# Performance work log

Hardware: AMD Instinct MI355X
Metric: run time of the kernel (lower is better)

The kernel has to match this reference:

```python
import jax, jax.numpy as jnp
import numpy as np

B, S, D = 32, 4096, 64          # batch, max seq len, input_dim
P, STRIDE, H = 8, 4, 512        # patch_size, patch_stride, hidden_size
T = (S - P) // STRIDE + 1       # static max token count (sample 0 has length S)
EPS = 1e-6


def setup_inputs() -> dict:
    key = jax.random.key(0)
    k1, k2, k3 = jax.random.split(key, 3)
    x = jax.random.normal(k1, (B, S, D), dtype=jnp.float32)
    lengths = jax.random.randint(k2, (B,), P, S + 1)
    lengths = lengths.at[0].set(S)  # at least one full-length sample -> max_tokens == T
    W = jax.random.normal(k3, (P * D, H), dtype=jnp.float32) / np.sqrt(P * D)
    b = jnp.zeros((H,), dtype=jnp.float32)
    scale = jnp.ones((H,), dtype=jnp.float32)  # RMSNorm scale
    return {"x": x, "lengths": lengths, "W": W, "b": b, "scale": scale}


def _patch(x, lengths):
    # number of tokens per sample: len(range(0, max(L-P+1, 1), STRIDE))
    n_tok = jnp.where(lengths >= P, (lengths - P) // STRIDE + 1, 1)  # [B]
    # gather positions for every (token, within-patch) slot
    pos = jnp.arange(T)[:, None] * STRIDE + jnp.arange(P)[None, :]   # [T, P]
    tokens = x[:, pos, :]                                            # [B, T, P, D]
    valid = (pos[None, :, :] < lengths[:, None, None]) \
          & (jnp.arange(T)[None, :, None] < n_tok[:, None, None])    # [B, T, P]
    tokens = jnp.where(valid[..., None], tokens, 0.0)
    return tokens.reshape(B, T, P * D), n_tok


def reference(x, lengths, W, b, scale):
    tokens, token_lengths = _patch(x, lengths)        # [B, T, P*D], [B]
    h = tokens @ W + b                                # proj -> [B, T, H]
    rms = jnp.sqrt(jnp.mean(h * h, axis=-1, keepdims=True) + EPS)
    hidden = h / rms * scale                          # RMSNorm
    return hidden, token_lengths, tokens
```

## Files before the change

kernel.cpp:

```cpp
#include <hip/hip_runtime.h>
#include <hip/hip_bf16.h>

constexpr int Bc = 32, Sc = 4096, Dc = 64, Pc = 8, STRIDEc = 4, Hc = 512;
constexpr int Tc = (Sc - Pc) / STRIDEc + 1;
constexpr int Kc = Pc * Dc;
constexpr float EPSc = 1e-6f;
constexpr int APITCH = 40;

typedef __bf16 bf16x8 __attribute__((ext_vector_type(8)));
typedef unsigned short ushort8 __attribute__((ext_vector_type(8)));
typedef float f32x4 __attribute__((ext_vector_type(4)));

__device__ __forceinline__ int n_tok_of(int len) {
    return (len >= Pc) ? ((len - Pc) / STRIDEc + 1) : 1;
}

__device__ __forceinline__ unsigned short f2bf(float f) {
    unsigned u = __builtin_bit_cast(unsigned, f);
    u = (u + 0x7FFFu + ((u >> 16) & 1u)) >> 16;
    return (unsigned short)u;
}
__device__ __forceinline__ unsigned pk2bf(float lo, float hi) {
    return (unsigned)f2bf(lo) | ((unsigned)f2bf(hi) << 16);
}

#define GLOAD_LDS16(gp, lp)                                                   \
    __builtin_amdgcn_global_load_lds(                                         \
        (const __attribute__((address_space(1))) void*)(gp),                  \
        (__attribute__((address_space(3))) void*)(lp), 16, 0, 0)

__global__ __launch_bounds__(256) void prep_kernel(
        const float* __restrict__ W, const int* __restrict__ lengths,
        unsigned short* __restrict__ Wfrag, float* __restrict__ out_tl) {
    __shared__ float tile[32][33];
    const int k0 = blockIdx.x * 32, n0 = blockIdx.y * 32;
    const int r = threadIdx.x >> 3, c = (threadIdx.x & 7) * 4;
    const float4 v = *(const float4*)(W + (size_t)(k0 + r) * Hc + n0 + c);
    tile[c + 0][r] = v.x;
    tile[c + 1][r] = v.y;
    tile[c + 2][r] = v.z;
    tile[c + 3][r] = v.w;
    __syncthreads();
    ushort4 o;
    o.x = f2bf(tile[r][c + 0]);
    o.y = f2bf(tile[r][c + 1]);
    o.z = f2bf(tile[r][c + 2]);
    o.w = f2bf(tile[r][c + 3]);
    const int n   = n0 + r;
    const int kk  = k0 + c;
    const int st  = kk >> 5;
    const int kg  = (kk >> 3) & 3;
    const int j   = kk & 7;
    const int slot = kg ^ ((n >> 1) & 3);
    const size_t off = (size_t)st * 16384 + (size_t)n * 32 + slot * 8 + j;
    *(ushort4*)(Wfrag + off) = o;
    if (blockIdx.x == 0 && blockIdx.y == 0 && threadIdx.x < Bc)
        out_tl[threadIdx.x] = (float)n_tok_of(lengths[threadIdx.x]);
}

__global__ __launch_bounds__(256) void fused_kernel(
        const float* __restrict__ x, const int* __restrict__ lengths,
        const unsigned short* __restrict__ Wfrag, const float* __restrict__ bias,
        const float* __restrict__ scale, float* __restrict__ hidden,
        float* __restrict__ tokens) {
    const int b  = blockIdx.y;
    const int t0 = blockIdx.x * 64;
    const int len = lengths[b];
    const int ntok = n_tok_of(len);

    __shared__ unsigned short As[64 * APITCH];
    __shared__ unsigned short Bs[512 * 32];
    __shared__ float ssbuf[4][64];

    const int tid  = threadIdx.x;
    const int w    = tid >> 6;
    const int lane = tid & 63;
    const int l15  = lane & 15;
    const int quad = lane >> 4;

    f32x4 acc[4][8];
#pragma unroll
    for (int tt = 0; tt < 4; ++tt)
#pragma unroll
        for (int ct = 0; ct < 8; ++ct) acc[tt][ct] = (f32x4){0.f, 0.f, 0.f, 0.f};

    const float* xb   = x + (size_t)b * (Sc * Dc);
    float*       tokb = tokens + (size_t)b * Tc * Kc;

    const unsigned short* a_rd[4];
#pragma unroll
    for (int tt = 0; tt < 4; ++tt)
        a_rd[tt] = As + (tt * 16 + l15) * APITCH + quad * 8;
    const unsigned short* b_rd[8];
#pragma unroll
    for (int ct = 0; ct < 8; ++ct) {
        const int n = w * 128 + ct * 16 + l15;
        b_rd[ct] = Bs + n * 32 + (quad ^ ((n >> 1) & 3)) * 8;
    }

    for (int step = 0; step < 16; ++step) {
        const int k0 = step * 32;
        if (step) __syncthreads();

#pragma unroll
        for (int it = 0; it < 2; ++it) {
            const int l = tid + it * 256;
            const int r = l >> 3;
            const int c = (l & 7) * 4;
            const int t = t0 + r;
            const int kk = k0 + c;
            const int pos = t * STRIDEc + (kk >> 6);
            float4 v = make_float4(0.f, 0.f, 0.f, 0.f);
            if (t < ntok && pos < len)
                v = *(const float4*)(xb + (size_t)t * (STRIDEc * Dc) + kk);
            if (t < Tc)
                *(float4*)(tokb + (size_t)t * Kc + kk) = v;
            ushort4 h4;
            h4.x = f2bf(v.x); h4.y = f2bf(v.y); h4.z = f2bf(v.z); h4.w = f2bf(v.w);
            *(ushort4*)(As + r * APITCH + c) = h4;
        }

        const unsigned short* wstep = Wfrag + (size_t)step * 16384;
#pragma unroll
        for (int it = 0; it < 8; ++it) {
            const int cc = w * 8 + it;
            GLOAD_LDS16(wstep + (size_t)cc * 512 + lane * 8, Bs + cc * 512);
        }
        __syncthreads();

        bf16x8 btok[4];
#pragma unroll
        for (int tt = 0; tt < 4; ++tt)
            btok[tt] = __builtin_bit_cast(bf16x8, *(const ushort8*)a_rd[tt]);
#pragma unroll
        for (int ct = 0; ct < 8; ++ct) {
            const bf16x8 av = __builtin_bit_cast(bf16x8, *(const ushort8*)b_rd[ct]);
#pragma unroll
            for (int tt = 0; tt < 4; ++tt)
                acc[tt][ct] = __builtin_amdgcn_mfma_f32_16x16x32_bf16(
                    av, btok[tt], acc[tt][ct], 0, 0, 0);
        }
    }

    float ss[4] = {0.f, 0.f, 0.f, 0.f};
#pragma unroll
    for (int ct = 0; ct < 8; ++ct) {
        const f32x4 b4 = *(const f32x4*)(bias + w * 128 + ct * 16 + quad * 4);
#pragma unroll
        for (int tt = 0; tt < 4; ++tt) {
            f32x4 h = acc[tt][ct] + b4;
            acc[tt][ct] = h;
            ss[tt] += h[0] * h[0] + h[1] * h[1] + h[2] * h[2] + h[3] * h[3];
        }
    }
#pragma unroll
    for (int tt = 0; tt < 4; ++tt) {
        float s = ss[tt];
        s += __shfl_xor(s, 16);
        s += __shfl_xor(s, 32);
        if (quad == 0) ssbuf[w][tt * 16 + l15] = s;
    }
    __syncthreads();
    float rstd[4];
#pragma unroll
    for (int tt = 0; tt < 4; ++tt) {
        const int r = tt * 16 + l15;
        const float tot = ssbuf[0][r] + ssbuf[1][r] + ssbuf[2][r] + ssbuf[3][r];
        rstd[tt] = rsqrtf(tot * (1.0f / (float)Hc) + EPSc);
    }
#pragma unroll
    for (int ct = 0; ct < 8; ++ct) {
        const f32x4 s4 = *(const f32x4*)(scale + w * 128 + ct * 16 + quad * 4);
#pragma unroll
        for (int tt = 0; tt < 4; ++tt) {
            const int t = t0 + tt * 16 + l15;
            if (t < Tc) {
                f32x4 o = acc[tt][ct] * rstd[tt] * s4;
                *(f32x4*)(hidden + ((size_t)b * Tc + t) * Hc
                          + w * 128 + ct * 16 + quad * 4) = o;
            }
        }
    }
}

extern "C" void kernel_launch(void* const* d_in, const int* in_sizes, int n_in,
                              void* d_out, int out_size, void* d_ws, size_t ws_size,
                              hipStream_t stream) {
    const float* x       = (const float*)d_in[0];
    const int*   lengths = (const int*)d_in[1];
    const float* W       = (const float*)d_in[2];
    const float* bias    = (const float*)d_in[3];
    const float* scale   = (const float*)d_in[4];

    const size_t BTH = (size_t)Bc * Tc * Hc;
    float* out    = (float*)d_out;
    float* hidden = out;
    float* tl     = out + BTH;
    float* tokens = out + BTH + Bc;

    unsigned short* Wfrag = (unsigned short*)d_ws;

    {
        dim3 grid(Hc / 32, Hc / 32);
        prep_kernel<<<grid, 256, 0, stream>>>(W, lengths, Wfrag, tl);
    }
    {
        dim3 grid(16, Bc);
        fused_kernel<<<grid, 256, 0, stream>>>(x, lengths, Wfrag, bias, scale,
                                               hidden, tokens);
    }
}
```

Measured before the change: 214.6 us.

## Halve token tile and register-prefetch next A/W stage during MFMA compute

Each block now handles 32 tokens instead of 64, doubling the grid and adding a launch-bounds occupancy hint. Loads of the next K-step's x slice and W fragments are moved into registers before the current step's MFMAs, then stored to LDS at the top of the next iteration. The direct global-to-LDS loads are replaced by this software prefetch. The aim is to hide global memory latency and raise occupancy. The cost is that each W stage is read once per 32 tokens instead of per 64, and the prefetched W fragments use more registers.

```diff
diff --git a/kernel.cpp b/kernel.cpp
--- a/kernel.cpp
+++ b/kernel.cpp
@@ -20,14 +20,6 @@
     u = (u + 0x7FFFu + ((u >> 16) & 1u)) >> 16;
     return (unsigned short)u;
 }
-__device__ __forceinline__ unsigned pk2bf(float lo, float hi) {
-    return (unsigned)f2bf(lo) | ((unsigned)f2bf(hi) << 16);
-}
-
-#define GLOAD_LDS16(gp, lp)                                                   \
-    __builtin_amdgcn_global_load_lds(                                         \
-        (const __attribute__((address_space(1))) void*)(gp),                  \
-        (__attribute__((address_space(3))) void*)(lp), 16, 0, 0)
 
 __global__ __launch_bounds__(256) void prep_kernel(
         const float* __restrict__ W, const int* __restrict__ lengths,
@@ -58,19 +50,19 @@
         out_tl[threadIdx.x] = (float)n_tok_of(lengths[threadIdx.x]);
 }
 
-__global__ __launch_bounds__(256) void fused_kernel(
+__global__ __launch_bounds__(256, 3) void fused_kernel(
         const float* __restrict__ x, const int* __restrict__ lengths,
         const unsigned short* __restrict__ Wfrag, const float* __restrict__ bias,
         const float* __restrict__ scale, float* __restrict__ hidden,
         float* __restrict__ tokens) {
     const int b  = blockIdx.y;
-    const int t0 = blockIdx.x * 64;
+    const int t0 = blockIdx.x * 32;
     const int len = lengths[b];
     const int ntok = n_tok_of(len);
 
-    __shared__ unsigned short As[64 * APITCH];
+    __shared__ unsigned short As[32 * APITCH];
     __shared__ unsigned short Bs[512 * 32];
-    __shared__ float ssbuf[4][64];
+    __shared__ float ssbuf[4][32];
 
     const int tid  = threadIdx.x;
     const int w    = tid >> 6;
@@ -78,18 +70,24 @@
     const int l15  = lane & 15;
     const int quad = lane >> 4;
 
-    f32x4 acc[4][8];
-#pragma unroll
-    for (int tt = 0; tt < 4; ++tt)
+    f32x4 acc[2][8];
+#pragma unroll
+    for (int tt = 0; tt < 2; ++tt)
 #pragma unroll
         for (int ct = 0; ct < 8; ++ct) acc[tt][ct] = (f32x4){0.f, 0.f, 0.f, 0.f};
 
     const float* xb   = x + (size_t)b * (Sc * Dc);
     float*       tokb = tokens + (size_t)b * Tc * Kc;
 
-    const unsigned short* a_rd[4];
-#pragma unroll
-    for (int tt = 0; tt < 4; ++tt)
+    const int a_r = tid >> 3;
+    const int a_c = (tid & 7) * 4;
+    const int a_t = t0 + a_r;
+    const bool a_tv = (a_t < Tc);
+    const float* a_src = xb + (size_t)a_t * (STRIDEc * Dc);
+
+    const unsigned short* a_rd[2];
+#pragma unroll
+    for (int tt = 0; tt < 2; ++tt)
         a_rd[tt] = As + (tt * 16 + l15) * APITCH + quad * 8;
     const unsigned short* b_rd[8];
 #pragma unroll
@@ -98,72 +96,82 @@
         b_rd[ct] = Bs + n * 32 + (quad ^ ((n >> 1) & 3)) * 8;
     }
 
+    float4  ra;
+    ushort8 rb[8];
+
+    {
+        const int pos = a_t * STRIDEc + (a_c >> 6);
+        ra = make_float4(0.f, 0.f, 0.f, 0.f);
+        if (a_t < ntok && pos < len) ra = *(const float4*)(a_src + a_c);
+#pragma unroll
+        for (int it = 0; it < 8; ++it)
+            rb[it] = *(const ushort8*)(Wfrag + (size_t)(tid + it * 256) * 8);
+    }
+
     for (int step = 0; step < 16; ++step) {
         const int k0 = step * 32;
         if (step) __syncthreads();
 
-#pragma unroll
-        for (int it = 0; it < 2; ++it) {
-            const int l = tid + it * 256;
-            const int r = l >> 3;
-            const int c = (l & 7) * 4;
-            const int t = t0 + r;
-            const int kk = k0 + c;
-            const int pos = t * STRIDEc + (kk >> 6);
-            float4 v = make_float4(0.f, 0.f, 0.f, 0.f);
-            if (t < ntok && pos < len)
-                v = *(const float4*)(xb + (size_t)t * (STRIDEc * Dc) + kk);
-            if (t < Tc)
-                *(float4*)(tokb + (size_t)t * Kc + kk) = v;
+        {
+            const float4 v = ra;
+            if (a_tv)
+                *(float4*)(tokb + (size_t)a_t * Kc + k0 + a_c) = v;
             ushort4 h4;
             h4.x = f2bf(v.x); h4.y = f2bf(v.y); h4.z = f2bf(v.z); h4.w = f2bf(v.w);
-            *(ushort4*)(As + r * APITCH + c) = h4;
-        }
-
-        const unsigned short* wstep = Wfrag + (size_t)step * 16384;
-#pragma unroll
-        for (int it = 0; it < 8; ++it) {
-            const int cc = w * 8 + it;
-            GLOAD_LDS16(wstep + (size_t)cc * 512 + lane * 8, Bs + cc * 512);
-        }
+            *(ushort4*)(As + a_r * APITCH + a_c) = h4;
+        }
+#pragma unroll
+        for (int it = 0; it < 8; ++it)
+            *(ushort8*)(Bs + (size_t)(tid + it * 256) * 8) = rb[it];
         __syncthreads();
 
-        bf16x8 btok[4];
-#pragma unroll
-        for (int tt = 0; tt < 4; ++tt)
+        if (step < 15) {
+            const int kn = k0 + 32 + a_c;
+            const int pos = a_t * STRIDEc + (kn >> 6);
+            ra = make_float4(0.f, 0.f, 0.f, 0.f);
+            if (a_t < ntok && pos < len) ra = *(const float4*)(a_src + kn);
+            const unsigned short* wsrc = Wfrag + (size_t)(step + 1) * 16384;
+#pragma unroll
+            for (int it = 0; it < 8; ++it)
+                rb[it] = *(const ushort8*)(wsrc + (size_t)(tid + it * 256) * 8);
+        }
+
+        bf16x8 btok[2];
+#pragma unroll
+        for (int tt = 0; tt < 2; ++tt)
             btok[tt] = __builtin_bit_cast(bf16x8, *(const ushort8*)a_rd[tt]);
 #pragma unroll
         for (int ct = 0; ct < 8; ++ct) {
             const bf16x8 av = __builtin_bit_cast(bf16x8, *(const ushort8*)b_rd[ct]);
 #pragma unroll
-            for (int tt = 0; tt < 4; ++tt)
+            for (int tt = 0; tt < 2; ++tt)
                 acc[tt][ct] = __builtin_amdgcn_mfma_f32_16x16x32_bf16(
                     av, btok[tt], acc[tt][ct], 0, 0, 0);
         }
     }
 
-    float ss[4] = {0.f, 0.f, 0.f, 0.f};
+    float ss[2] = {0.f, 0.f};
 #pragma unroll
     for (int ct = 0; ct < 8; ++ct) {
         const f32x4 b4 = *(const f32x4*)(bias + w * 128 + ct * 16 + quad * 4);
 #pragma unroll
-        for (int tt = 0; tt < 4; ++tt) {
+        for (int tt = 0; tt < 2; ++tt) {
             f32x4 h = acc[tt][ct] + b4;
             acc[tt][ct] = h;
             ss[tt] += h[0] * h[0] + h[1] * h[1] + h[2] * h[2] + h[3] * h[3];
         }
     }
 #pragma unroll
-    for (int tt = 0; tt < 4; ++tt) {
+    for (int tt = 0; tt < 2; ++tt) {
         float s = ss[tt];
         s += __shfl_xor(s, 16);
         s += __shfl_xor(s, 32);
         if (quad == 0) ssbuf[w][tt * 16 + l15] = s;
     }
     __syncthreads();
-    float rstd[4];
-#pragma unroll
-    for (int tt = 0; tt < 4; ++tt) {
+    float rstd[2];
+#pragma unroll
+    for (int tt = 0; tt < 2; ++tt) {
         const int r = tt * 16 + l15;
         const float tot = ssbuf[0][r] + ssbuf[1][r] + ssbuf[2][r] + ssbuf[3][r];
         rstd[tt] = rsqrtf(tot * (1.0f / (float)Hc) + EPSc);
@@ -172,7 +180,7 @@
     for (int ct = 0; ct < 8; ++ct) {
         const f32x4 s4 = *(const f32x4*)(scale + w * 128 + ct * 16 + quad * 4);
 #pragma unroll
-        for (int tt = 0; tt < 4; ++tt) {
+        for (int tt = 0; tt < 2; ++tt) {
             const int t = t0 + tt * 16 + l15;
             if (t < Tc) {
                 f32x4 o = acc[tt][ct] * rstd[tt] * s4;
@@ -205,7 +213,7 @@
         prep_kernel<<<grid, 256, 0, stream>>>(W, lengths, Wfrag, tl);
     }
     {
-        dim3 grid(16, Bc);
+        dim3 grid(32, Bc);
         fused_kernel<<<grid, 256, 0, stream>>>(x, lengths, Wfrag, bias, scale,
                                                hidden, tokens);
     }
```

Result: faster. 200.0 us (-6.8%).
